# Kernel optimization log

Hardware: AMD Instinct MI355X
Metric: run time of the kernel (lower is better)

The kernel has to match this reference:

```python
import jax, jax.numpy as jnp
import numpy as np


def setup_inputs() -> dict:
    key = jax.random.key(0)
    ks = jax.random.split(key, 5)
    B, in_ch, H, W = 8, 256, 128, 128
    C = in_ch // 4
    x = jax.random.normal(ks[0], (B, in_ch, H, W), dtype=jnp.float32)
    # 1x1 conv weights stored as [out_ch, in_ch] (kernel spatial dims are 1)
    w_in = jax.random.normal(ks[1], (C, in_ch), dtype=jnp.float32) * (1.0 / np.sqrt(in_ch))
    b_in = jax.random.normal(ks[2], (C,), dtype=jnp.float32) * 0.01
    w_out = jax.random.normal(ks[3], (in_ch, C), dtype=jnp.float32) * (1.0 / np.sqrt(C))
    b_out = jax.random.normal(ks[4], (in_ch,), dtype=jnp.float32) * 0.01
    detal = jnp.array([0.1], dtype=jnp.float32)
    return {"x": x, "w_in": w_in, "b_in": b_in, "w_out": w_out, "b_out": b_out, "detal": detal}


def _mda(x, w_in, b_in, w_out, b_out, detal):
    # InConv: 1x1 conv == channel GEMM
    inp = jnp.einsum('bihw,oi->bohw', x, w_in) + b_in[None, :, None, None]
    B, C, H, W = inp.shape

    # ---- W branch ----
    # AdaptiveAvgPool2d((None,1)) -> mean over W; softmax over size-1 axis (== ones, kept for faithfulness)
    f_w = jax.nn.softmax(inp.mean(axis=3, keepdims=True), axis=3)          # [B,C,H,1]
    f_w = jnp.transpose(f_w, (0, 3, 1, 2)).reshape(B, C * H, 1)
    Xw = inp.reshape(B, C * H, W)
    Gw = Xw * f_w                                                          # [B,CH,W]
    Tw = jax.nn.softmax(jnp.einsum('bkw,bkv->bwv', Gw, Gw), axis=1)        # [B,W,W], softmax over rows
    Wo = jnp.einsum('bkw,bwv->bkv', Xw, Tw).reshape(B, C, H, W)

    # ---- H branch ----
    f_h = jax.nn.softmax(jnp.transpose(inp, (0, 1, 3, 2)).mean(axis=3, keepdims=True), axis=3)  # [B,C,W,1]
    f_h = jnp.transpose(f_h, (0, 3, 1, 2)).reshape(B, C * W, 1)
    Xh = inp.reshape(B, C * W, H)  # raw .view as in torch (scrambles H/W axes intentionally)
    Gh = Xh * f_h
    Th = jax.nn.softmax(jnp.einsum('bkh,bkg->bhg', Gh, Gh), axis=1)        # [B,H,H]
    Ho = jnp.einsum('bkh,bhg->bkg', Xh, Th).reshape(B, C, H, W)

    # ---- C branch ----
    perm = jnp.transpose(inp, (0, 2, 3, 1))                                # [B,H,W,C]
    f_c = jax.nn.softmax(perm.mean(axis=3, keepdims=True), axis=3)         # [B,H,W,1]
    f_c = jnp.transpose(f_c, (0, 3, 1, 2)).reshape(B, H * W, 1)
    Xc = perm.reshape(B, H * W, C)
    Gc = f_c * Xc
    Tc = jax.nn.softmax(jnp.einsum('bnc,bnd->bcd', Gc, Gc), axis=1)        # [B,C,C]
    # torch does .view(B,C,H,W) on a [B,H*W,C] tensor: raw reshape, NOT a transpose
    Co = jnp.einsum('bnc,bcd->bnd', Xc, Tc).reshape(B, C, H, W)

    s = detal[0] * (Co + Wo + Ho)
    # OuConv 1x1 + residual
    return jnp.einsum('bchw,oc->bohw', s, w_out) + b_out[None, :, None, None] + x


def reference(x, w_in, b_in, w_out, b_out, detal):
    return _mda(x, w_in, b_in, w_out, b_out, detal)
```

## Files before the change

kernel.cpp:

```cpp
#include <hip/hip_runtime.h>
#include <math.h>

#define NB 8
#define IC 256
#define CC 64
#define HH 128
#define WW 128
#define NN (HH*WW)
#define NKW 64
#define NKC 64

typedef _Float16 f16x8 __attribute__((ext_vector_type(8)));
typedef float f32x4 __attribute__((ext_vector_type(4)));

static constexpr size_t SZ_INP  = (size_t)NB * CC * NN;
static constexpr size_t OFF_INP = 0;
static constexpr size_t OFF_S   = OFF_INP + SZ_INP;
static constexpr size_t OFF_PC  = OFF_S + SZ_INP;
static constexpr size_t OFF_TW  = OFF_PC + (size_t)NB * NKC * 4096;
static constexpr size_t OFF_TC  = OFF_TW + (size_t)NB * 16384;
static constexpr size_t OFF_WT  = OFF_TC + (size_t)NB * 4096;
static constexpr size_t OFF_WOT = OFF_WT + 16384;

__global__ __launch_bounds__(256) void k_wt(
    const float* __restrict__ w_in, const float* __restrict__ w_out,
    _Float16* __restrict__ wh, _Float16* __restrict__ woh)
{
    const int idx = blockIdx.x * 256 + threadIdx.x;
    if (idx < 16384) wh[idx] = (_Float16)w_in[idx];
    else             woh[idx - 16384] = (_Float16)w_out[idx - 16384];
}

__global__ __launch_bounds__(256) void k_inconv(
    const float* __restrict__ x, const _Float16* __restrict__ wh,
    const float* __restrict__ b_in, float* __restrict__ inp)
{
    __shared__ _Float16 wl[64 * 264];
    __shared__ _Float16 xh[32 * 136];
    const int b  = blockIdx.y;
    const int n0 = blockIdx.x * 128;
    const int t  = threadIdx.x;
    const int l  = t & 63, wv = t >> 6;
    const int lr = l & 15, kg = (l >> 4) * 8;

    {
        const int r = t >> 2, c = (t & 3) * 64;
        const uint4* src = (const uint4*)(wh + r * 256 + c);
        uint4* dst = (uint4*)(wl + r * 264 + c);
#pragma unroll
        for (int k = 0; k < 8; k++) dst[k] = src[k];
    }

    f32x4 acc[4][2];
#pragma unroll
    for (int mt = 0; mt < 4; mt++)
#pragma unroll
        for (int nt = 0; nt < 2; nt++) acc[mt][nt] = (f32x4){0.f, 0.f, 0.f, 0.f};

    for (int kc = 0; kc < 8; ++kc) {
        __syncthreads();
        {
            const int i = t >> 3, nq = (t & 7) * 16;
            const float* src = x + ((size_t)b * IC + kc * 32 + i) * NN + n0 + nq;
            const float4 v0 = *(const float4*)(src);
            const float4 v1 = *(const float4*)(src + 4);
            const float4 v2 = *(const float4*)(src + 8);
            const float4 v3 = *(const float4*)(src + 12);
            f16x8 h0, h1;
            h0[0] = (_Float16)v0.x; h0[1] = (_Float16)v0.y;
            h0[2] = (_Float16)v0.z; h0[3] = (_Float16)v0.w;
            h0[4] = (_Float16)v1.x; h0[5] = (_Float16)v1.y;
            h0[6] = (_Float16)v1.z; h0[7] = (_Float16)v1.w;
            h1[0] = (_Float16)v2.x; h1[1] = (_Float16)v2.y;
            h1[2] = (_Float16)v2.z; h1[3] = (_Float16)v2.w;
            h1[4] = (_Float16)v3.x; h1[5] = (_Float16)v3.y;
            h1[6] = (_Float16)v3.z; h1[7] = (_Float16)v3.w;
            *(f16x8*)(xh + i * 136 + nq)     = h0;
            *(f16x8*)(xh + i * 136 + nq + 8) = h1;
        }
        __syncthreads();

        f16x8 bf[2];
#pragma unroll
        for (int nt = 0; nt < 2; ++nt) {
            const int n = wv * 32 + nt * 16 + lr;
#pragma unroll
            for (int j = 0; j < 8; ++j) bf[nt][j] = xh[(kg + j) * 136 + n];
        }
#pragma unroll
        for (int mt = 0; mt < 4; ++mt) {
            const f16x8 af = *(const f16x8*)(wl + (mt * 16 + lr) * 264 + kc * 32 + kg);
            acc[mt][0] = __builtin_amdgcn_mfma_f32_16x16x32_f16(af, bf[0], acc[mt][0], 0, 0, 0);
            acc[mt][1] = __builtin_amdgcn_mfma_f32_16x16x32_f16(af, bf[1], acc[mt][1], 0, 0, 0);
        }
    }

#pragma unroll
    for (int mt = 0; mt < 4; ++mt)
#pragma unroll
        for (int nt = 0; nt < 2; ++nt) {
            const int n = n0 + wv * 32 + nt * 16 + lr;
#pragma unroll
            for (int r = 0; r < 4; ++r) {
                const int o = mt * 16 + (l >> 4) * 4 + r;
                inp[((size_t)b * CC + o) * NN + n] = (float)acc[mt][nt][r] + b_in[o];
            }
        }
}

__global__ __launch_bounds__(256) void k_gramW(const float* __restrict__ inp, float* __restrict__ pW)
{
    __shared__ float xs[32 * 132];
    const int b = blockIdx.y, kc = blockIdx.x;
    const int t = threadIdx.x, tx = t & 15, ty = t >> 4;
    const float* Xb = inp + (size_t)b * CC * NN;
    const int k0 = kc * ((CC * HH) / NKW);

    float acc[8][8];
#pragma unroll
    for (int i = 0; i < 8; i++)
#pragma unroll
        for (int j = 0; j < 8; j++) acc[i][j] = 0.f;

    for (int kk = k0; kk < k0 + (CC * HH) / NKW; kk += 32) {
        __syncthreads();
        {
            const int r = t >> 3, cq = (t & 7) * 16;
            const float* src = Xb + ((size_t)kk + r) * WW + cq;
            float* dst = xs + r * 132 + cq;
#pragma unroll
            for (int j = 0; j < 4; j++)
                *(float4*)(dst + 4 * j) = *(const float4*)(src + 4 * j);
        }
        __syncthreads();
#pragma unroll 8
        for (int k = 0; k < 32; k++) {
            const float* row = xs + k * 132;
            float4 t0 = *(const float4*)(row + ty * 8);
            float4 t1 = *(const float4*)(row + ty * 8 + 4);
            float4 u0 = *(const float4*)(row + tx * 8);
            float4 u1 = *(const float4*)(row + tx * 8 + 4);
            float av[8] = {t0.x, t0.y, t0.z, t0.w, t1.x, t1.y, t1.z, t1.w};
            float bv[8] = {u0.x, u0.y, u0.z, u0.w, u1.x, u1.y, u1.z, u1.w};
#pragma unroll
            for (int i = 0; i < 8; i++)
#pragma unroll
                for (int j = 0; j < 8; j++) acc[i][j] += av[i] * bv[j];
        }
    }
    float* dst = pW + ((size_t)b * NKW + kc) * 16384;
#pragma unroll
    for (int i = 0; i < 8; i++)
#pragma unroll
        for (int j = 0; j < 8; j += 4) {
            float4 v = make_float4(acc[i][j], acc[i][j + 1], acc[i][j + 2], acc[i][j + 3]);
            *(float4*)(dst + (ty * 8 + i) * 128 + tx * 8 + j) = v;
        }
}

__global__ __launch_bounds__(256) void k_redW(const float* __restrict__ pW, float* __restrict__ Tw)
{
    const int b = blockIdx.y;
    const int idx = blockIdx.x * 256 + threadIdx.x;
    const float* p = pW + (size_t)b * NKW * 16384 + idx;
    float acc = 0.f;
#pragma unroll
    for (int k = 0; k < NKW; k++) acc += p[(size_t)k * 16384];
    Tw[(size_t)b * 16384 + idx] = acc;
}

__global__ __launch_bounds__(1024) void k_softW(float* __restrict__ Tw)
{
    __shared__ float red[32 * 33];
    const int b = blockIdx.x, v0 = blockIdx.y * 32;
    const int t = threadIdx.x;
    const int vc = t & 31, wg = t >> 5;
    float* S = Tw + (size_t)b * 16384 + v0 + vc;

    float v[4];
    float m = -3.4e38f;
#pragma unroll
    for (int j = 0; j < 4; j++) { v[j] = S[(wg * 4 + j) * 128]; m = fmaxf(m, v[j]); }
    red[wg * 33 + vc] = m;
    __syncthreads();
    for (int st = 16; st > 0; st >>= 1) {
        if (wg < st) red[wg * 33 + vc] = fmaxf(red[wg * 33 + vc], red[(wg + st) * 33 + vc]);
        __syncthreads();
    }
    m = red[vc];
    __syncthreads();
    float sum = 0.f;
#pragma unroll
    for (int j = 0; j < 4; j++) { v[j] = __expf(v[j] - m); sum += v[j]; }
    red[wg * 33 + vc] = sum;
    __syncthreads();
    for (int st = 16; st > 0; st >>= 1) {
        if (wg < st) red[wg * 33 + vc] += red[(wg + st) * 33 + vc];
        __syncthreads();
    }
    const float inv = 1.f / red[vc];
#pragma unroll
    for (int j = 0; j < 4; j++) S[(wg * 4 + j) * 128] = v[j] * inv;
}

__global__ __launch_bounds__(256) void k_gramC(const float* __restrict__ inp, float* __restrict__ pC)
{
    __shared__ float xt[32 * 68];
    const int b = blockIdx.y, nc = blockIdx.x;
    const int t = threadIdx.x, tx = t & 15, ty = t >> 4;
    const float* ip = inp + (size_t)b * CC * NN;
    const int n0 = nc * (NN / NKC);

    float acc[4][4];
#pragma unroll
    for (int i = 0; i < 4; i++)
#pragma unroll
        for (int j = 0; j < 4; j++) acc[i][j] = 0.f;

    const int scc = t >> 2;
    const int sn  = (t & 3) * 8;

    for (int nt = 0; nt < NN / NKC; nt += 32) {
        __syncthreads();
        {
            const float* src = ip + (size_t)scc * NN + n0 + nt + sn;
            float v[8];
            *(float4*)(v)     = *(const float4*)(src);
            *(float4*)(v + 4) = *(const float4*)(src + 4);
#pragma unroll
            for (int j = 0; j < 8; j++) xt[(sn + j) * 68 + scc] = v[j];
        }
        __syncthreads();
#pragma unroll 8
        for (int nn = 0; nn < 32; nn++) {
            const float4 a4 = *(const float4*)(xt + nn * 68 + ty * 4);
            const float4 e4 = *(const float4*)(xt + nn * 68 + tx * 4);
            const float av[4] = {a4.x, a4.y, a4.z, a4.w};
            const float ev[4] = {e4.x, e4.y, e4.z, e4.w};
#pragma unroll
            for (int i = 0; i < 4; i++)
#pragma unroll
                for (int j = 0; j < 4; j++) acc[i][j] += av[i] * ev[j];
        }
    }
    float* dst = pC + ((size_t)b * NKC + nc) * 4096;
#pragma unroll
    for (int i = 0; i < 4; i++) {
        float4 v = make_float4(acc[i][0], acc[i][1], acc[i][2], acc[i][3]);
        *(float4*)(dst + (ty * 4 + i) * 64 + tx * 4) = v;
    }
}

__global__ __launch_bounds__(256) void k_redC(const float* __restrict__ pC, float* __restrict__ Tc)
{
    const int b = blockIdx.y;
    const int idx = blockIdx.x * 256 + threadIdx.x;
    const float* p = pC + (size_t)b * NKC * 4096 + idx;
    float acc = 0.f;
#pragma unroll
    for (int k = 0; k < NKC; k++) acc += p[(size_t)k * 4096];
    Tc[(size_t)b * 4096 + idx] = acc;
}

__global__ __launch_bounds__(1024) void k_softC(float* __restrict__ Tc)
{
    __shared__ float red[16 * 65];
    const int b = blockIdx.x;
    const int t = threadIdx.x;
    const int dc = t & 63, cg = t >> 6;
    float* S = Tc + (size_t)b * 4096 + dc;

    float v[4];
    float m = -3.4e38f;
#pragma unroll
    for (int j = 0; j < 4; j++) { v[j] = S[(cg * 4 + j) * 64]; m = fmaxf(m, v[j]); }
    red[cg * 65 + dc] = m;
    __syncthreads();
    for (int st = 8; st > 0; st >>= 1) {
        if (cg < st) red[cg * 65 + dc] = fmaxf(red[cg * 65 + dc], red[(cg + st) * 65 + dc]);
        __syncthreads();
    }
    m = red[dc];
    __syncthreads();
    float sum = 0.f;
#pragma unroll
    for (int j = 0; j < 4; j++) { v[j] = __expf(v[j] - m); sum += v[j]; }
    red[cg * 65 + dc] = sum;
    __syncthreads();
    for (int st = 8; st > 0; st >>= 1) {
        if (cg < st) red[cg * 65 + dc] += red[(cg + st) * 65 + dc];
        __syncthreads();
    }
    const float inv = 1.f / red[dc];
#pragma unroll
    for (int j = 0; j < 4; j++) S[(cg * 4 + j) * 64] = v[j] * inv;
}

__global__ __launch_bounds__(256) void k_co(
    const float* __restrict__ inp, const float* __restrict__ Tc,
    const float* __restrict__ detal, float* __restrict__ s)
{
    __shared__ float tc[64 * 68];
    __shared__ float xs[64 * 132];
    const int b  = blockIdx.y;
    const int n0 = blockIdx.x * 128;
    const int t  = threadIdx.x;
    const int d4 = (t & 15) * 4;
    const int g8 = (t >> 4) * 8;

    {
        const int sr = t >> 2, sc = (t & 3) * 4;
        const float* src = inp + ((size_t)b * CC + sr) * NN + n0;
        float* dst = xs + sr * 132;
#pragma unroll
        for (int k = 0; k < 8; k++)
            *(float4*)(dst + sc + 16 * k) = *(const float4*)(src + sc + 16 * k);
        const float* tsrc = Tc + (size_t)b * 4096 + sr * 64;
        float* tdst = tc + sr * 68;
#pragma unroll
        for (int k = 0; k < 4; k++)
            *(float4*)(tdst + sc + 16 * k) = *(const float4*)(tsrc + sc + 16 * k);
    }
    __syncthreads();

    float acc[8][4];
#pragma unroll
    for (int i = 0; i < 8; i++)
#pragma unroll
        for (int j = 0; j < 4; j++) acc[i][j] = 0.f;

#pragma unroll 4
    for (int c = 0; c < 64; c++) {
        const float4 t4 = *(const float4*)(tc + c * 68 + d4);
        const float4 xa = *(const float4*)(xs + c * 132 + g8);
        const float4 xb = *(const float4*)(xs + c * 132 + g8 + 4);
        const float xv[8] = {xa.x, xa.y, xa.z, xa.w, xb.x, xb.y, xb.z, xb.w};
        const float tv[4] = {t4.x, t4.y, t4.z, t4.w};
#pragma unroll
        for (int i = 0; i < 8; i++)
#pragma unroll
            for (int j = 0; j < 4; j++) acc[i][j] += xv[i] * tv[j];
    }
    const float scl = detal[0];
    float* sb = s + (size_t)b * CC * NN + (size_t)n0 * 64;
#pragma unroll
    for (int i = 0; i < 8; i++) {
        float4 v = make_float4(acc[i][0] * scl, acc[i][1] * scl,
                               acc[i][2] * scl, acc[i][3] * scl);
        *(float4*)(sb + (size_t)(g8 + i) * 64 + d4) = v;
    }
}

__global__ __launch_bounds__(128) void k_wo(
    const float* __restrict__ inp, const float* __restrict__ Tw,
    const float* __restrict__ detal, float* __restrict__ s)
{
    __shared__ float xt[32 * 68];
    __shared__ float twl[32 * 132];
    const int b = blockIdx.z, hc = blockIdx.y, c = blockIdx.x;
    const int t = threadIdx.x;
    const int rg = t >> 4;
    const int vg = t & 15;
    const int h0 = hc * 64;

    const float* ip = inp + ((size_t)b * CC + c) * NN + (size_t)h0 * WW;
    const float* twg = Tw + (size_t)b * 16384;

    float acc[8][8];
#pragma unroll
    for (int p = 0; p < 8; p++)
#pragma unroll
        for (int q = 0; q < 8; q++) acc[p][q] = 0.f;

    for (int w0 = 0; w0 < 128; w0 += 32) {
        __syncthreads();
        {
            const int h = t >> 1, wq = (t & 1) * 16;
            const float* src = ip + (size_t)h * WW + w0 + wq;
            float v[16];
            *(float4*)(v)      = *(const float4*)(src);
            *(float4*)(v + 4)  = *(const float4*)(src + 4);
            *(float4*)(v + 8)  = *(const float4*)(src + 8);
            *(float4*)(v + 12) = *(const float4*)(src + 12);
#pragma unroll
            for (int j = 0; j < 16; j++) xt[(wq + j) * 68 + h] = v[j];
        }
        {
            const int w = t >> 2, cq = (t & 3) * 32;
            const float* src = twg + (size_t)(w0 + w) * 128 + cq;
            float* dst = twl + w * 132 + cq;
#pragma unroll
            for (int k = 0; k < 8; k++)
                *(float4*)(dst + 4 * k) = *(const float4*)(src + 4 * k);
        }
        __syncthreads();
#pragma unroll 4
        for (int w = 0; w < 32; ++w) {
            const float4 ra = *(const float4*)(xt + w * 68 + rg * 8);
            const float4 rb = *(const float4*)(xt + w * 68 + rg * 8 + 4);
            const float4 ta = *(const float4*)(twl + w * 132 + vg * 4);
            const float4 tb = *(const float4*)(twl + w * 132 + 64 + vg * 4);
            const float rv[8] = {ra.x, ra.y, ra.z, ra.w, rb.x, rb.y, rb.z, rb.w};
            const float tv[8] = {ta.x, ta.y, ta.z, ta.w, tb.x, tb.y, tb.z, tb.w};
#pragma unroll
            for (int p = 0; p < 8; p++)
#pragma unroll
                for (int q = 0; q < 8; q++) acc[p][q] += rv[p] * tv[q];
        }
    }

    const float sc2 = 2.0f * detal[0];
    float* sp = s + ((size_t)b * CC + c) * NN + (size_t)h0 * WW;
#pragma unroll
    for (int p = 0; p < 8; ++p) {
        const int h = rg * 8 + p;
        float* q0 = sp + (size_t)h * WW + vg * 4;
        float* q1 = sp + (size_t)h * WW + 64 + vg * 4;
        float4 c0 = *(const float4*)q0;
        float4 c1 = *(const float4*)q1;
        c0.x += sc2 * acc[p][0]; c0.y += sc2 * acc[p][1];
        c0.z += sc2 * acc[p][2]; c0.w += sc2 * acc[p][3];
        c1.x += sc2 * acc[p][4]; c1.y += sc2 * acc[p][5];
        c1.z += sc2 * acc[p][6]; c1.w += sc2 * acc[p][7];
        *(float4*)q0 = c0;
        *(float4*)q1 = c1;
    }
}

__global__ __launch_bounds__(256) void k_outconv(
    const float* __restrict__ s, const _Float16* __restrict__ woh,
    const float* __restrict__ b_out, const float* __restrict__ x,
    float* __restrict__ outp)
{
    __shared__ _Float16 wo[256 * 72];
    __shared__ _Float16 sh[32 * 72];
    const int b  = blockIdx.y;
    const int n0 = blockIdx.x * 64;
    const int t  = threadIdx.x;
    const int l  = t & 63, wv = t >> 6;
    const int lr = l & 15, kg = (l >> 4) * 8;

    {
        const uint4* src = (const uint4*)(woh + t * 64);
        uint4* dst = (uint4*)(wo + t * 72);
#pragma unroll
        for (int k = 0; k < 4; k++) dst[k] = src[k];
        const uint4* src2 = src + 4;
        uint4* dst2 = dst + 4;
#pragma unroll
        for (int k = 0; k < 4; k++) dst2[k] = src2[k];
    }

    f32x4 acc[4][4];
#pragma unroll
    for (int mt = 0; mt < 4; mt++)
#pragma unroll
        for (int nt = 0; nt < 4; nt++) acc[mt][nt] = (f32x4){0.f, 0.f, 0.f, 0.f};

    for (int kc = 0; kc < 2; ++kc) {
        __syncthreads();
        {
            const int c = t >> 3, n8 = (t & 7) * 8;
            const float* src = s + ((size_t)b * CC + kc * 32 + c) * NN + n0 + n8;
            const float4 v0 = *(const float4*)(src);
            const float4 v1 = *(const float4*)(src + 4);
            f16x8 h;
            h[0] = (_Float16)v0.x; h[1] = (_Float16)v0.y;
            h[2] = (_Float16)v0.z; h[3] = (_Float16)v0.w;
            h[4] = (_Float16)v1.x; h[5] = (_Float16)v1.y;
            h[6] = (_Float16)v1.z; h[7] = (_Float16)v1.w;
            *(f16x8*)(sh + c * 72 + n8) = h;
        }
        __syncthreads();

        f16x8 bf[4];
#pragma unroll
        for (int nt = 0; nt < 4; ++nt) {
            const int n = nt * 16 + lr;
#pragma unroll
            for (int j = 0; j < 8; ++j) bf[nt][j] = sh[(kg + j) * 72 + n];
        }
#pragma unroll
        for (int mt = 0; mt < 4; ++mt) {
            const f16x8 af = *(const f16x8*)(wo + (wv * 64 + mt * 16 + lr) * 72 + kc * 32 + kg);
#pragma unroll
            for (int nt = 0; nt < 4; ++nt)
                acc[mt][nt] = __builtin_amdgcn_mfma_f32_16x16x32_f16(af, bf[nt], acc[mt][nt], 0, 0, 0);
        }
    }

#pragma unroll
    for (int mt = 0; mt < 4; ++mt)
#pragma unroll
        for (int nt = 0; nt < 4; ++nt) {
            const int n = n0 + nt * 16 + lr;
#pragma unroll
            for (int r = 0; r < 4; ++r) {
                const int o = wv * 64 + mt * 16 + (l >> 4) * 4 + r;
                const size_t off = ((size_t)b * IC + o) * NN + n;
                outp[off] = (float)acc[mt][nt][r] + b_out[o] + x[off];
            }
        }
}

extern "C" void kernel_launch(void* const* d_in, const int* in_sizes, int n_in,
                              void* d_out, int out_size, void* d_ws, size_t ws_size,
                              hipStream_t stream)
{
    const float* x     = (const float*)d_in[0];
    const float* w_in  = (const float*)d_in[1];
    const float* b_in  = (const float*)d_in[2];
    const float* w_out = (const float*)d_in[3];
    const float* b_out = (const float*)d_in[4];
    const float* detal = (const float*)d_in[5];
    float* out = (float*)d_out;

    float* ws   = (float*)d_ws;
    float* inp  = ws + OFF_INP;
    float* s    = ws + OFF_S;
    float* pW   = ws + OFF_S;
    float* pC   = ws + OFF_PC;
    float* Tw   = ws + OFF_TW;
    float* Tc   = ws + OFF_TC;
    _Float16* wh  = (_Float16*)(ws + OFF_WT);
    _Float16* woh = (_Float16*)(ws + OFF_WOT);

    k_wt     <<<dim3(128),              256, 0, stream>>>(w_in, w_out, wh, woh);
    k_inconv <<<dim3(NN / 128, NB),     256, 0, stream>>>(x, wh, b_in, inp);
    k_gramW  <<<dim3(NKW, NB),          256, 0, stream>>>(inp, pW);
    k_redW   <<<dim3(64, NB),           256, 0, stream>>>(pW, Tw);
    k_softW  <<<dim3(NB, 4),           1024, 0, stream>>>(Tw);
    k_gramC  <<<dim3(NKC, NB),          256, 0, stream>>>(inp, pC);
    k_redC   <<<dim3(16, NB),           256, 0, stream>>>(pC, Tc);
    k_softC  <<<dim3(NB),              1024, 0, stream>>>(Tc);
    k_co     <<<dim3(NN / 128, NB),     256, 0, stream>>>(inp, Tc, detal, s);
    k_wo     <<<dim3(CC, 2, NB),        128, 0, stream>>>(inp, Tw, detal, s);
    k_outconv<<<dim3(NN / 64, NB),      256, 0, stream>>>(s, woh, b_out, x, out);
}
```

Before: 445.2 us.

## Move Co and Wo apply GEMMs to fp16 MFMA with transposed fp16 attention maps

```diff
diff --git a/kernel.cpp b/kernel.cpp
--- a/kernel.cpp
+++ b/kernel.cpp
@@ -21,6 +21,8 @@
 static constexpr size_t OFF_TC  = OFF_TW + (size_t)NB * 16384;
 static constexpr size_t OFF_WT  = OFF_TC + (size_t)NB * 4096;
 static constexpr size_t OFF_WOT = OFF_WT + 16384;
+static constexpr size_t OFF_TWT = OFF_WOT + 16384;
+static constexpr size_t OFF_TCT = OFF_TWT + 65536;
 
 __global__ __launch_bounds__(256) void k_wt(
     const float* __restrict__ w_in, const float* __restrict__ w_out,
@@ -35,8 +37,8 @@
     const float* __restrict__ x, const _Float16* __restrict__ wh,
     const float* __restrict__ b_in, float* __restrict__ inp)
 {
-    __shared__ _Float16 wl[64 * 264];
-    __shared__ _Float16 xh[32 * 136];
+    __shared__ __align__(16) _Float16 wl[64 * 264];
+    __shared__ __align__(16) _Float16 xh[32 * 136];
     const int b  = blockIdx.y;
     const int n0 = blockIdx.x * 128;
     const int t  = threadIdx.x;
@@ -169,13 +171,13 @@
     Tw[(size_t)b * 16384 + idx] = acc;
 }
 
-__global__ __launch_bounds__(1024) void k_softW(float* __restrict__ Tw)
+__global__ __launch_bounds__(1024) void k_softW(const float* __restrict__ Tw, _Float16* __restrict__ twt)
 {
     __shared__ float red[32 * 33];
     const int b = blockIdx.x, v0 = blockIdx.y * 32;
     const int t = threadIdx.x;
     const int vc = t & 31, wg = t >> 5;
-    float* S = Tw + (size_t)b * 16384 + v0 + vc;
+    const float* S = Tw + (size_t)b * 16384 + v0 + vc;
 
     float v[4];
     float m = -3.4e38f;
@@ -199,8 +201,9 @@
         __syncthreads();
     }
     const float inv = 1.f / red[vc];
-#pragma unroll
-    for (int j = 0; j < 4; j++) S[(wg * 4 + j) * 128] = v[j] * inv;
+    _Float16* dst = twt + (size_t)b * 16384 + (size_t)(v0 + vc) * 128 + wg * 4;
+#pragma unroll
+    for (int j = 0; j < 4; j++) dst[j] = (_Float16)(v[j] * inv);
 }
 
 __global__ __launch_bounds__(256) void k_gramC(const float* __restrict__ inp, float* __restrict__ pC)
@@ -262,13 +265,13 @@
     Tc[(size_t)b * 4096 + idx] = acc;
 }
 
-__global__ __launch_bounds__(1024) void k_softC(float* __restrict__ Tc)
+__global__ __launch_bounds__(1024) void k_softC(const float* __restrict__ Tc, _Float16* __restrict__ tct)
 {
     __shared__ float red[16 * 65];
     const int b = blockIdx.x;
     const int t = threadIdx.x;
     const int dc = t & 63, cg = t >> 6;
-    float* S = Tc + (size_t)b * 4096 + dc;
+    const float* S = Tc + (size_t)b * 4096 + dc;
 
     float v[4];
     float m = -3.4e38f;
@@ -292,138 +295,144 @@
         __syncthreads();
     }
     const float inv = 1.f / red[dc];
-#pragma unroll
-    for (int j = 0; j < 4; j++) S[(cg * 4 + j) * 64] = v[j] * inv;
+    _Float16* dst = tct + (size_t)b * 4096 + (size_t)dc * 64 + cg * 4;
+#pragma unroll
+    for (int j = 0; j < 4; j++) dst[j] = (_Float16)(v[j] * inv);
 }
 
 __global__ __launch_bounds__(256) void k_co(
-    const float* __restrict__ inp, const float* __restrict__ Tc,
+    const float* __restrict__ inp, const _Float16* __restrict__ tct,
     const float* __restrict__ detal, float* __restrict__ s)
 {
-    __shared__ float tc[64 * 68];
-    __shared__ float xs[64 * 132];
+    __shared__ __align__(16) _Float16 xh[128 * 72];
+    __shared__ __align__(16) _Float16 tl[64 * 72];
     const int b  = blockIdx.y;
     const int n0 = blockIdx.x * 128;
     const int t  = threadIdx.x;
-    const int d4 = (t & 15) * 4;
-    const int g8 = (t >> 4) * 8;
+    const int l  = t & 63, wv = t >> 6;
+    const int lr = l & 15, kg = (l >> 4) * 8;
 
     {
-        const int sr = t >> 2, sc = (t & 3) * 4;
-        const float* src = inp + ((size_t)b * CC + sr) * NN + n0;
-        float* dst = xs + sr * 132;
-#pragma unroll
-        for (int k = 0; k < 8; k++)
-            *(float4*)(dst + sc + 16 * k) = *(const float4*)(src + sc + 16 * k);
-        const float* tsrc = Tc + (size_t)b * 4096 + sr * 64;
-        float* tdst = tc + sr * 68;
-#pragma unroll
-        for (int k = 0; k < 4; k++)
-            *(float4*)(tdst + sc + 16 * k) = *(const float4*)(tsrc + sc + 16 * k);
-    }
-    __syncthreads();
-
-    float acc[8][4];
-#pragma unroll
-    for (int i = 0; i < 8; i++)
-#pragma unroll
-        for (int j = 0; j < 4; j++) acc[i][j] = 0.f;
-
-#pragma unroll 4
-    for (int c = 0; c < 64; c++) {
-        const float4 t4 = *(const float4*)(tc + c * 68 + d4);
-        const float4 xa = *(const float4*)(xs + c * 132 + g8);
-        const float4 xb = *(const float4*)(xs + c * 132 + g8 + 4);
-        const float xv[8] = {xa.x, xa.y, xa.z, xa.w, xb.x, xb.y, xb.z, xb.w};
-        const float tv[4] = {t4.x, t4.y, t4.z, t4.w};
-#pragma unroll
-        for (int i = 0; i < 8; i++)
-#pragma unroll
-            for (int j = 0; j < 4; j++) acc[i][j] += xv[i] * tv[j];
-    }
+        const int nn = t & 127, ch = t >> 7;
+        const float* src = inp + ((size_t)b * CC + ch * 32) * NN + n0 + nn;
+#pragma unroll
+        for (int k2 = 0; k2 < 4; ++k2) {
+            float f[8];
+#pragma unroll
+            for (int j = 0; j < 8; ++j) f[j] = src[(size_t)(k2 * 8 + j) * NN];
+            f16x8 h;
+#pragma unroll
+            for (int j = 0; j < 8; ++j) h[j] = (_Float16)f[j];
+            *(f16x8*)(xh + nn * 72 + ch * 32 + k2 * 8) = h;
+        }
+    }
+    {
+        const int d = t >> 2, cq = (t & 3) * 16;
+        const _Float16* src = tct + (size_t)b * 4096 + d * 64 + cq;
+        *(uint4*)(tl + d * 72 + cq)     = *(const uint4*)(src);
+        *(uint4*)(tl + d * 72 + cq + 8) = *(const uint4*)(src + 8);
+    }
+    __syncthreads();
+
+    f32x4 acc[2][4];
+#pragma unroll
+    for (int mt = 0; mt < 2; mt++)
+#pragma unroll
+        for (int nt = 0; nt < 4; nt++) acc[mt][nt] = (f32x4){0.f, 0.f, 0.f, 0.f};
+
+#pragma unroll
+    for (int kc = 0; kc < 2; ++kc) {
+        f16x8 bf[4];
+#pragma unroll
+        for (int nt = 0; nt < 4; ++nt)
+            bf[nt] = *(const f16x8*)(tl + (nt * 16 + lr) * 72 + kc * 32 + kg);
+#pragma unroll
+        for (int mt = 0; mt < 2; ++mt) {
+            const f16x8 af = *(const f16x8*)(xh + (wv * 32 + mt * 16 + lr) * 72 + kc * 32 + kg);
+#pragma unroll
+            for (int nt = 0; nt < 4; ++nt)
+                acc[mt][nt] = __builtin_amdgcn_mfma_f32_16x16x32_f16(af, bf[nt], acc[mt][nt], 0, 0, 0);
+        }
+    }
+
     const float scl = detal[0];
-    float* sb = s + (size_t)b * CC * NN + (size_t)n0 * 64;
-#pragma unroll
-    for (int i = 0; i < 8; i++) {
-        float4 v = make_float4(acc[i][0] * scl, acc[i][1] * scl,
-                               acc[i][2] * scl, acc[i][3] * scl);
-        *(float4*)(sb + (size_t)(g8 + i) * 64 + d4) = v;
-    }
-}
-
-__global__ __launch_bounds__(128) void k_wo(
-    const float* __restrict__ inp, const float* __restrict__ Tw,
+    float* sb = s + (size_t)b * CC * NN;
+#pragma unroll
+    for (int mt = 0; mt < 2; ++mt)
+#pragma unroll
+        for (int nt = 0; nt < 4; ++nt) {
+            const int d = nt * 16 + lr;
+#pragma unroll
+            for (int r = 0; r < 4; ++r) {
+                const int n = n0 + wv * 32 + mt * 16 + (l >> 4) * 4 + r;
+                sb[(size_t)n * 64 + d] = scl * acc[mt][nt][r];
+            }
+        }
+}
+
+__global__ __launch_bounds__(256) void k_wo(
+    const float* __restrict__ inp, const _Float16* __restrict__ twt,
     const float* __restrict__ detal, float* __restrict__ s)
 {
-    __shared__ float xt[32 * 68];
-    __shared__ float twl[32 * 132];
+    __shared__ __align__(16) _Float16 xh[64 * 136];
+    __shared__ __align__(16) _Float16 tl[128 * 136];
     const int b = blockIdx.z, hc = blockIdx.y, c = blockIdx.x;
     const int t = threadIdx.x;
-    const int rg = t >> 4;
-    const int vg = t & 15;
+    const int l = t & 63, wv = t >> 6;
+    const int lr = l & 15, kg = (l >> 4) * 8;
     const int h0 = hc * 64;
 
     const float* ip = inp + ((size_t)b * CC + c) * NN + (size_t)h0 * WW;
-    const float* twg = Tw + (size_t)b * 16384;
-
-    float acc[8][8];
-#pragma unroll
-    for (int p = 0; p < 8; p++)
-#pragma unroll
-        for (int q = 0; q < 8; q++) acc[p][q] = 0.f;
-
-    for (int w0 = 0; w0 < 128; w0 += 32) {
-        __syncthreads();
-        {
-            const int h = t >> 1, wq = (t & 1) * 16;
-            const float* src = ip + (size_t)h * WW + w0 + wq;
-            float v[16];
-            *(float4*)(v)      = *(const float4*)(src);
-            *(float4*)(v + 4)  = *(const float4*)(src + 4);
-            *(float4*)(v + 8)  = *(const float4*)(src + 8);
-            *(float4*)(v + 12) = *(const float4*)(src + 12);
-#pragma unroll
-            for (int j = 0; j < 16; j++) xt[(wq + j) * 68 + h] = v[j];
-        }
-        {
-            const int w = t >> 2, cq = (t & 3) * 32;
-            const float* src = twg + (size_t)(w0 + w) * 128 + cq;
-            float* dst = twl + w * 132 + cq;
-#pragma unroll
-            for (int k = 0; k < 8; k++)
-                *(float4*)(dst + 4 * k) = *(const float4*)(src + 4 * k);
-        }
-        __syncthreads();
-#pragma unroll 4
-        for (int w = 0; w < 32; ++w) {
-            const float4 ra = *(const float4*)(xt + w * 68 + rg * 8);
-            const float4 rb = *(const float4*)(xt + w * 68 + rg * 8 + 4);
-            const float4 ta = *(const float4*)(twl + w * 132 + vg * 4);
-            const float4 tb = *(const float4*)(twl + w * 132 + 64 + vg * 4);
-            const float rv[8] = {ra.x, ra.y, ra.z, ra.w, rb.x, rb.y, rb.z, rb.w};
-            const float tv[8] = {ta.x, ta.y, ta.z, ta.w, tb.x, tb.y, tb.z, tb.w};
-#pragma unroll
-            for (int p = 0; p < 8; p++)
-#pragma unroll
-                for (int q = 0; q < 8; q++) acc[p][q] += rv[p] * tv[q];
+
+    {
+        const int h = t >> 2, wq = (t & 3) * 32;
+        const float* src = ip + (size_t)h * WW + wq;
+#pragma unroll
+        for (int k2 = 0; k2 < 4; ++k2) {
+            const float4 v0 = *(const float4*)(src + k2 * 8);
+            const float4 v1 = *(const float4*)(src + k2 * 8 + 4);
+            f16x8 h8;
+            h8[0] = (_Float16)v0.x; h8[1] = (_Float16)v0.y;
+            h8[2] = (_Float16)v0.z; h8[3] = (_Float16)v0.w;
+            h8[4] = (_Float16)v1.x; h8[5] = (_Float16)v1.y;
+            h8[6] = (_Float16)v1.z; h8[7] = (_Float16)v1.w;
+            *(f16x8*)(xh + h * 136 + wq + k2 * 8) = h8;
+        }
+    }
+    {
+        const int v = t >> 1, wh2 = (t & 1) * 64;
+        const _Float16* src = twt + (size_t)b * 16384 + (size_t)v * 128 + wh2;
+        uint4* dst = (uint4*)(tl + v * 136 + wh2);
+#pragma unroll
+        for (int k = 0; k < 8; ++k) dst[k] = *(const uint4*)(src + 8 * k);
+    }
+    __syncthreads();
+
+    f32x4 acc[8];
+#pragma unroll
+    for (int nt = 0; nt < 8; nt++) acc[nt] = (f32x4){0.f, 0.f, 0.f, 0.f};
+
+#pragma unroll
+    for (int kc = 0; kc < 4; ++kc) {
+        const f16x8 af = *(const f16x8*)(xh + (wv * 16 + lr) * 136 + kc * 32 + kg);
+#pragma unroll
+        for (int nt = 0; nt < 8; ++nt) {
+            const f16x8 bf = *(const f16x8*)(tl + (nt * 16 + lr) * 136 + kc * 32 + kg);
+            acc[nt] = __builtin_amdgcn_mfma_f32_16x16x32_f16(af, bf, acc[nt], 0, 0, 0);
         }
     }
 
     const float sc2 = 2.0f * detal[0];
     float* sp = s + ((size_t)b * CC + c) * NN + (size_t)h0 * WW;
 #pragma unroll
-    for (int p = 0; p < 8; ++p) {
-        const int h = rg * 8 + p;
-        float* q0 = sp + (size_t)h * WW + vg * 4;
-        float* q1 = sp + (size_t)h * WW + 64 + vg * 4;
-        float4 c0 = *(const float4*)q0;
-        float4 c1 = *(const float4*)q1;
-        c0.x += sc2 * acc[p][0]; c0.y += sc2 * acc[p][1];
-        c0.z += sc2 * acc[p][2]; c0.w += sc2 * acc[p][3];
-        c1.x += sc2 * acc[p][4]; c1.y += sc2 * acc[p][5];
-        c1.z += sc2 * acc[p][6]; c1.w += sc2 * acc[p][7];
-        *(float4*)q0 = c0;
-        *(float4*)q1 = c1;
+    for (int nt = 0; nt < 8; ++nt) {
+        const int v = nt * 16 + lr;
+#pragma unroll
+        for (int r = 0; r < 4; ++r) {
+            const int h = wv * 16 + (l >> 4) * 4 + r;
+            float* p = sp + (size_t)h * WW + v;
+            *p = *p + sc2 * acc[nt][r];
+        }
     }
 }
 
@@ -432,8 +441,8 @@
     const float* __restrict__ b_out, const float* __restrict__ x,
     float* __restrict__ outp)
 {
-    __shared__ _Float16 wo[256 * 72];
-    __shared__ _Float16 sh[32 * 72];
+    __shared__ __align__(16) _Float16 wo[256 * 72];
+    __shared__ __align__(16) _Float16 sh[32 * 72];
     const int b  = blockIdx.y;
     const int n0 = blockIdx.x * 64;
     const int t  = threadIdx.x;
@@ -444,11 +453,7 @@
         const uint4* src = (const uint4*)(woh + t * 64);
         uint4* dst = (uint4*)(wo + t * 72);
 #pragma unroll
-        for (int k = 0; k < 4; k++) dst[k] = src[k];
-        const uint4* src2 = src + 4;
-        uint4* dst2 = dst + 4;
-#pragma unroll
-        for (int k = 0; k < 4; k++) dst2[k] = src2[k];
+        for (int k = 0; k < 8; k++) dst[k] = src[k];
     }
 
     f32x4 acc[4][4];
@@ -524,16 +529,18 @@
     float* Tc   = ws + OFF_TC;
     _Float16* wh  = (_Float16*)(ws + OFF_WT);
     _Float16* woh = (_Float16*)(ws + OFF_WOT);
+    _Float16* twt = (_Float16*)(ws + OFF_TWT);
+    _Float16* tct = (_Float16*)(ws + OFF_TCT);
 
     k_wt     <<<dim3(128),              256, 0, stream>>>(w_in, w_out, wh, woh);
     k_inconv <<<dim3(NN / 128, NB),     256, 0, stream>>>(x, wh, b_in, inp);
     k_gramW  <<<dim3(NKW, NB),          256, 0, stream>>>(inp, pW);
     k_redW   <<<dim3(64, NB),           256, 0, stream>>>(pW, Tw);
-    k_softW  <<<dim3(NB, 4),           1024, 0, stream>>>(Tw);
+    k_softW  <<<dim3(NB, 4),           1024, 0, stream>>>(Tw, twt);
     k_gramC  <<<dim3(NKC, NB),          256, 0, stream>>>(inp, pC);
     k_redC   <<<dim3(16, NB),           256, 0, stream>>>(pC, Tc);
-    k_softC  <<<dim3(NB),              1024, 0, stream>>>(Tc);
-    k_co     <<<dim3(NN / 128, NB),     256, 0, stream>>>(inp, Tc, detal, s);
-    k_wo     <<<dim3(CC, 2, NB),        128, 0, stream>>>(inp, Tw, detal, s);
+    k_softC  <<<dim3(NB),              1024, 0, stream>>>(Tc, tct);
+    k_co     <<<dim3(NN / 128, NB),     256, 0, stream>>>(inp, tct, detal, s);
+    k_wo     <<<dim3(CC, 2, NB),        256, 0, stream>>>(inp, twt, detal, s);
     k_outconv<<<dim3(NN / 64, NB),      256, 0, stream>>>(s, woh, b_out, x, out);
 }
```

After: 413.7 us. 1.08x faster.
